# Optimization experiments

Measured on AMD Instinct MI355X. Metric: run time of the kernel, lower is better.

Reference implementation:

```python
import jax, jax.numpy as jnp
import numpy as np

EPS = 1e-08

def setup_inputs() -> dict:
    key = jax.random.key(0)
    x = jax.random.normal(key, (8192,), dtype=jnp.float32)
    return {"x": x}

def reference(x):
    xf = x.reshape(-1)
    n = xf.shape[0]
    min_x = jnp.min(xf)
    # shift so all values are non-negative only when min is negative (matches torch branch)
    xf = jnp.where(min_x < 0, xf - min_x, xf)
    mu = jnp.mean(xf) + EPS
    # explicit O(n^2) pairwise abs-diff sum, same math as the torch module
    sum_diff = jnp.sum(jnp.abs(xf[None, :] - xf[:, None]))
    gini = sum_diff / (2.0 * (n * n) * mu)
    return gini
```

## Files before the change

### kernel.cpp

```cpp
#include <hip/hip_runtime.h>


#define EPS 1e-8f

__global__ void __launch_bounds__(256) gini_pair_partial(
    const float* __restrict__ x, float* __restrict__ partials, int n) {
    __shared__ __align__(16) float sm[8192];
    for (int i = threadIdx.x; i < n; i += 256) sm[i] = x[i];
    __syncthreads();

    int g   = blockIdx.x * 256 + threadIdx.x;
    int row = g >> 3;
    int seg = g & 7;
    float acc = 0.0f;
    if (row < n) {
        float xi = sm[row];
        const float4* sm4 = (const float4*)sm;
        int nchunks = n >> 2;
        for (int c = seg; c < nchunks; c += 8) {
            float4 v = sm4[c];
            acc += fabsf(xi - v.x);
            acc += fabsf(xi - v.y);
            acc += fabsf(xi - v.z);
            acc += fabsf(xi - v.w);
        }
    }
    #pragma unroll
    for (int off = 32; off > 0; off >>= 1) acc += __shfl_down(acc, off, 64);
    __shared__ float wsum[4];
    int wave = threadIdx.x >> 6;
    if ((threadIdx.x & 63) == 0) wsum[wave] = acc;
    __syncthreads();
    if (threadIdx.x == 0)
        partials[blockIdx.x] = wsum[0] + wsum[1] + wsum[2] + wsum[3];
}

__global__ void __launch_bounds__(256) gini_finalize(
    const float* __restrict__ x, const float* __restrict__ partials,
    int nblocks, float* __restrict__ out, int n) {
    float lmin = 3.4e38f, lsum = 0.0f, psum = 0.0f;
    for (int i = threadIdx.x; i < n; i += 256) {
        float v = x[i];
        lmin = fminf(lmin, v);
        lsum += v;
    }
    for (int i = threadIdx.x; i < nblocks; i += 256) psum += partials[i];

    #pragma unroll
    for (int off = 32; off > 0; off >>= 1) {
        lmin = fminf(lmin, __shfl_down(lmin, off, 64));
        lsum += __shfl_down(lsum, off, 64);
        psum += __shfl_down(psum, off, 64);
    }
    __shared__ float smin[4], ssum[4], spsum[4];
    int wave = threadIdx.x >> 6;
    if ((threadIdx.x & 63) == 0) {
        smin[wave] = lmin; ssum[wave] = lsum; spsum[wave] = psum;
    }
    __syncthreads();
    if (threadIdx.x == 0) {
        float mn = fminf(fminf(smin[0], smin[1]), fminf(smin[2], smin[3]));
        float sum = ssum[0] + ssum[1] + ssum[2] + ssum[3];
        float sd  = spsum[0] + spsum[1] + spsum[2] + spsum[3];
        float shifted_sum = (mn < 0.0f) ? (sum - (float)n * mn) : sum;
        float mu = shifted_sum / (float)n + EPS;
        out[0] = sd / (2.0f * (float)n * (float)n * mu);
    }
}

extern "C" void kernel_launch(void* const* d_in, const int* in_sizes, int n_in,
                              void* d_out, int out_size, void* d_ws, size_t ws_size,
                              hipStream_t stream) {
    const float* x = (const float*)d_in[0];
    float* out = (float*)d_out;
    float* partials = (float*)d_ws;
    int n = in_sizes[0];

    int nblocks = (n * 8 + 255) / 256;
    gini_pair_partial<<<nblocks, 256, 0, stream>>>(x, partials, n);
    gini_finalize<<<1, 256, 0, stream>>>(x, partials, nblocks, out, n);
}
```

Baseline: 72.17 us.

## Register-block 8 rows per thread and vectorize LDS staging

Each thread now holds 8 row values in registers and sweeps a strided slice of columns, so each float4 LDS read feeds 32 abs-diffs instead of 4. Staging into shared memory uses float4 loads. The grid doubles to 512 blocks, which doubles the redundant per-block copies of the input into LDS, and the accumulation order changes.

After: 64.51 us. -10.6%, faster.

```diff
diff --git a/kernel.cpp b/kernel.cpp
--- a/kernel.cpp
+++ b/kernel.cpp
@@ -6,25 +6,42 @@
 __global__ void __launch_bounds__(256) gini_pair_partial(
     const float* __restrict__ x, float* __restrict__ partials, int n) {
     __shared__ __align__(16) float sm[8192];
-    for (int i = threadIdx.x; i < n; i += 256) sm[i] = x[i];
+    const int nchunks = n >> 2;
+    {
+        const float4* xv = (const float4*)x;
+        float4* smv = (float4*)sm;
+        for (int i = threadIdx.x; i < nchunks; i += 256) smv[i] = xv[i];
+    }
     __syncthreads();
 
-    int g   = blockIdx.x * 256 + threadIdx.x;
-    int row = g >> 3;
-    int seg = g & 7;
-    float acc = 0.0f;
-    if (row < n) {
-        float xi = sm[row];
+    int g     = blockIdx.x * 256 + threadIdx.x;
+    int group = g >> 7;
+    int seg   = g & 127;
+    int row0  = group * 8;
+
+    float acc0 = 0.f, acc1 = 0.f, acc2 = 0.f, acc3 = 0.f;
+    float acc4 = 0.f, acc5 = 0.f, acc6 = 0.f, acc7 = 0.f;
+    if (row0 + 7 < n) {
+        float r0 = sm[row0 + 0], r1 = sm[row0 + 1];
+        float r2 = sm[row0 + 2], r3 = sm[row0 + 3];
+        float r4 = sm[row0 + 4], r5 = sm[row0 + 5];
+        float r6 = sm[row0 + 6], r7 = sm[row0 + 7];
         const float4* sm4 = (const float4*)sm;
-        int nchunks = n >> 2;
-        for (int c = seg; c < nchunks; c += 8) {
+        #pragma unroll 4
+        for (int c = seg; c < nchunks; c += 128) {
             float4 v = sm4[c];
-            acc += fabsf(xi - v.x);
-            acc += fabsf(xi - v.y);
-            acc += fabsf(xi - v.z);
-            acc += fabsf(xi - v.w);
+            acc0 += (fabsf(r0 - v.x) + fabsf(r0 - v.y)) + (fabsf(r0 - v.z) + fabsf(r0 - v.w));
+            acc1 += (fabsf(r1 - v.x) + fabsf(r1 - v.y)) + (fabsf(r1 - v.z) + fabsf(r1 - v.w));
+            acc2 += (fabsf(r2 - v.x) + fabsf(r2 - v.y)) + (fabsf(r2 - v.z) + fabsf(r2 - v.w));
+            acc3 += (fabsf(r3 - v.x) + fabsf(r3 - v.y)) + (fabsf(r3 - v.z) + fabsf(r3 - v.w));
+            acc4 += (fabsf(r4 - v.x) + fabsf(r4 - v.y)) + (fabsf(r4 - v.z) + fabsf(r4 - v.w));
+            acc5 += (fabsf(r5 - v.x) + fabsf(r5 - v.y)) + (fabsf(r5 - v.z) + fabsf(r5 - v.w));
+            acc6 += (fabsf(r6 - v.x) + fabsf(r6 - v.y)) + (fabsf(r6 - v.z) + fabsf(r6 - v.w));
+            acc7 += (fabsf(r7 - v.x) + fabsf(r7 - v.y)) + (fabsf(r7 - v.z) + fabsf(r7 - v.w));
         }
     }
+    float acc = ((acc0 + acc1) + (acc2 + acc3)) + ((acc4 + acc5) + (acc6 + acc7));
+
     #pragma unroll
     for (int off = 32; off > 0; off >>= 1) acc += __shfl_down(acc, off, 64);
     __shared__ float wsum[4];
@@ -32,7 +49,7 @@
     if ((threadIdx.x & 63) == 0) wsum[wave] = acc;
     __syncthreads();
     if (threadIdx.x == 0)
-        partials[blockIdx.x] = wsum[0] + wsum[1] + wsum[2] + wsum[3];
+        partials[blockIdx.x] = (wsum[0] + wsum[1]) + (wsum[2] + wsum[3]);
 }
 
 __global__ void __launch_bounds__(256) gini_finalize(
@@ -59,9 +76,9 @@
     }
     __syncthreads();
     if (threadIdx.x == 0) {
-        float mn = fminf(fminf(smin[0], smin[1]), fminf(smin[2], smin[3]));
-        float sum = ssum[0] + ssum[1] + ssum[2] + ssum[3];
-        float sd  = spsum[0] + spsum[1] + spsum[2] + spsum[3];
+        float mn  = fminf(fminf(smin[0], smin[1]), fminf(smin[2], smin[3]));
+        float sum = (ssum[0] + ssum[1]) + (ssum[2] + ssum[3]);
+        float sd  = (spsum[0] + spsum[1]) + (spsum[2] + spsum[3]);
         float shifted_sum = (mn < 0.0f) ? (sum - (float)n * mn) : sum;
         float mu = shifted_sum / (float)n + EPS;
         out[0] = sd / (2.0f * (float)n * (float)n * mu);
@@ -76,7 +93,7 @@
     float* partials = (float*)d_ws;
     int n = in_sizes[0];
 
-    int nblocks = (n * 8 + 255) / 256;
+    int nblocks = (n * 16 + 255) / 256;
     gini_pair_partial<<<nblocks, 256, 0, stream>>>(x, partials, n);
     gini_finalize<<<1, 256, 0, stream>>>(x, partials, nblocks, out, n);
 }
```
